# Performance work log

Measured on AMD Instinct MI355X. Metric: run time of the kernel, lower is better.

The kernel has to match this reference:

```python
import jax, jax.numpy as jnp
import numpy as np

B, S, E, H = 8, 512, 1024, 16
D = E // H  # head_dim = 64


def _rope_tables(seq_len, head_dim):
    inv_freq = 1.0 / (10000.0 ** (np.arange(0, head_dim, 2, dtype=np.float32) / head_dim))
    pos = np.arange(seq_len, dtype=np.float32)
    ang = np.einsum('i,j->ij', pos, inv_freq)  # [S, D/2]
    return jnp.asarray(np.cos(ang)), jnp.asarray(np.sin(ang))


def setup_inputs() -> dict:
    key = jax.random.key(0)
    ks = jax.random.split(key, 12)
    std = 1.0 / np.sqrt(E)
    inp = {
        'x_q': jax.random.normal(ks[0], (B, S, E), jnp.float32),
        'x_k': jax.random.normal(ks[1], (B, S, E), jnp.float32),
        'x_v': jax.random.normal(ks[2], (B, S, E), jnp.float32),
        'Wq': jax.random.normal(ks[3], (E, E), jnp.float32) * std,
        'bq': jnp.zeros((E,), jnp.float32),
        'Wk': jax.random.normal(ks[4], (E, E), jnp.float32) * std,
        'bk': jnp.zeros((E,), jnp.float32),
        'Wv': jax.random.normal(ks[5], (E, E), jnp.float32) * std,
        'bv': jnp.zeros((E,), jnp.float32),
        'Wo': jax.random.normal(ks[6], (E, E), jnp.float32) * std,
        'bo': jnp.zeros((E,), jnp.float32),
        'temperature': jnp.ones((), jnp.float32),
    }
    cos, sin = _rope_tables(S, D)
    inp['cos'] = cos
    inp['sin'] = sin
    return inp


def reference(x_q, x_k, x_v, Wq, bq, Wk, bk, Wv, bv, Wo, bo, temperature, cos, sin):
    b, s, e = x_q.shape
    h, d = H, D

    def proj(x, W, bias):
        # torch Linear: x @ W.T + b ; then split heads -> [b, h, s, d]
        y = jnp.einsum('bse,fe->bsf', x, W) + bias
        return y.reshape(b, s, h, d).transpose(0, 2, 1, 3)

    q = proj(x_q, Wq, bq)
    k = proj(x_k, Wk, bk)
    v = proj(x_v, Wv, bv)

    c = cos[:s]  # [s, d/2]
    sn = sin[:s]

    def rope(t):
        # interleaved pairing: view as [..., d/2, 2]
        t2 = t.reshape(b, h, s, d // 2, 2)
        t0, t1 = t2[..., 0], t2[..., 1]
        r = jnp.stack([t0 * c - t1 * sn, t0 * sn + t1 * c], axis=-1)
        return r.reshape(b, h, s, d)

    q = rope(q)
    k = rope(k)

    def l2norm(t):
        # torch F.normalize: x / max(||x||, eps)
        n = jnp.sqrt(jnp.sum(t * t, axis=-1, keepdims=True))
        return t / jnp.maximum(n, 1e-12)

    q = l2norm(q)
    k = l2norm(k)

    scores = jnp.einsum('bhqd,bhkd->bhqk', q, k) * temperature
    attn = jax.nn.softmax(scores, axis=-1)
    out = jnp.einsum('bhqk,bhkd->bhqd', attn, v)
    out = out.transpose(0, 2, 1, 3).reshape(b, s, e)
    return jnp.einsum('bse,fe->bsf', out, Wo) + bo
```

## Files before the change

kernel.cpp:

```cpp
#include <hip/hip_runtime.h>
#include <stdint.h>

#define DEV __device__ __forceinline__

typedef __bf16 bf16x8 __attribute__((ext_vector_type(8)));
typedef float f32x4 __attribute__((ext_vector_type(4)));
typedef unsigned short u16;
typedef u16 u16x8 __attribute__((ext_vector_type(8)));
typedef u16 u16x4 __attribute__((ext_vector_type(4)));
typedef __attribute__((address_space(3))) uint8_t lds8;
typedef __attribute__((address_space(1))) const uint8_t glb8;

constexpr int Bb = 8, Ss = 512, Ee = 1024, Hh = 16;
constexpr int BS = Bb * Ss;

DEV u16 f2bf(float f) {
  union { float f; uint32_t u; } v; v.f = f;
  return (u16)((v.u + 0x7FFFu + ((v.u >> 16) & 1u)) >> 16);
}
DEV bf16x8 ldsbf8(const u16* p) {
  u16x8 u = *(const u16x8*)p;
  return __builtin_bit_cast(bf16x8, u);
}
DEV f32x4 mfma16(bf16x8 a, bf16x8 b, f32x4 c) {
  return __builtin_amdgcn_mfma_f32_16x16x32_bf16(a, b, c, 0, 0, 0);
}

struct ConvArgs {
  const float* s[7];
  u16* d[7];
  int n[7];
};

__global__ __launch_bounds__(256) void convert_k(ConvArgs a) {
  int z = blockIdx.y;
  int base = (blockIdx.x * 256 + threadIdx.x) * 8;
  if (base >= a.n[z]) return;
  const float4* sp = (const float4*)(a.s[z] + base);
  float4 v0 = sp[0], v1 = sp[1];
  u16x8 o;
  o[0] = f2bf(v0.x); o[1] = f2bf(v0.y); o[2] = f2bf(v0.z); o[3] = f2bf(v0.w);
  o[4] = f2bf(v1.x); o[5] = f2bf(v1.y); o[6] = f2bf(v1.z); o[7] = f2bf(v1.w);
  *(u16x8*)(a.d[z] + base) = o;
}

DEV void gemm_main(const u16* __restrict__ A, const u16* __restrict__ W,
                   f32x4 (&acc)[4][4]) {
  constexpr int K = Ee;
  __shared__ u16 sA[2][128 * 32], sB[2][128 * 32];
  const int tid = threadIdx.x, lane = tid & 63, wid = tid >> 6;
  const int lr = lane & 15, lh = lane >> 4;
  const int m0 = blockIdx.x * 128, n0 = blockIdx.y * 128;
  const int wm = (wid >> 1) * 64, wn = (wid & 1) * 64;

  const u16* aSrc[2]; const u16* bSrc[2]; int ldsOff[2];
#pragma unroll
  for (int j = 0; j < 2; ++j) {
    int c0 = j * 256 + wid * 64;
    int c = c0 + lane;
    int q = c >> 3, sl = c & 7;
    int rp = sl ^ (q & 7);
    int r = q * 2 + (rp >> 2), p = rp & 3;
    aSrc[j] = A + (size_t)(m0 + r) * K + p * 8;
    bSrc[j] = W + (size_t)(n0 + r) * K + p * 8;
    ldsOff[j] = c0 * 8;
  }
  int offA[4], offB[4];
#pragma unroll
  for (int t = 0; t < 4; ++t) {
    int ra = wm + t * 16 + lr;
    offA[t] = (ra >> 1) * 64 + ((((ra & 1) << 2) | lh) ^ ((ra >> 1) & 7)) * 8;
    int rb = wn + t * 16 + lr;
    offB[t] = (rb >> 1) * 64 + ((((rb & 1) << 2) | lh) ^ ((rb >> 1) & 7)) * 8;
  }
#pragma unroll
  for (int a = 0; a < 4; ++a)
#pragma unroll
    for (int q = 0; q < 4; ++q) acc[a][q] = f32x4{0.f, 0.f, 0.f, 0.f};

#define GSTAGE(buf, k0_)                                                       \
  {                                                                            \
    _Pragma("unroll") for (int j = 0; j < 2; ++j) {                            \
      __builtin_amdgcn_global_load_lds((glb8*)(aSrc[j] + (k0_)),               \
                                       (lds8*)&sA[buf][ldsOff[j]], 16, 0, 0);  \
      __builtin_amdgcn_global_load_lds((glb8*)(bSrc[j] + (k0_)),               \
                                       (lds8*)&sB[buf][ldsOff[j]], 16, 0, 0);  \
    }                                                                          \
  }

  GSTAGE(0, 0);
  __syncthreads();
  int cur = 0;
  for (int k0 = 0; k0 < K; k0 += 32) {
    if (k0 + 32 < K) GSTAGE(cur ^ 1, k0 + 32);
    bf16x8 af[4], bfv[4];
#pragma unroll
    for (int t = 0; t < 4; ++t) {
      af[t] = ldsbf8(&sA[cur][offA[t]]);
      bfv[t] = ldsbf8(&sB[cur][offB[t]]);
    }
#pragma unroll
    for (int mt = 0; mt < 4; ++mt)
#pragma unroll
      for (int nt = 0; nt < 4; ++nt)
        acc[mt][nt] = mfma16(af[mt], bfv[nt], acc[mt][nt]);
    __syncthreads();
    cur ^= 1;
  }
#undef GSTAGE
}

__global__ __launch_bounds__(256) void gemm_qkv(
    const u16* xq, const u16* xk, const u16* xv,
    const u16* wq, const u16* wk, const u16* wv,
    const float* bq_, const float* bk_, const float* bv_,
    const float* __restrict__ cosT, const float* __restrict__ sinT,
    u16* qh, u16* kh, u16* vt) {
  int z = blockIdx.z;
  const u16* A = z == 0 ? xq : (z == 1 ? xk : xv);
  const u16* W = z == 0 ? wq : (z == 1 ? wk : wv);
  const float* bias = z == 0 ? bq_ : (z == 1 ? bk_ : bv_);
  f32x4 acc[4][4];
  gemm_main(A, W, acc);

  const int tid = threadIdx.x, lane = tid & 63, wid = tid >> 6;
  const int lr = lane & 15, lh = lane >> 4;
  const int m0 = blockIdx.x * 128, n0 = blockIdx.y * 128;
  const int wm = (wid >> 1) * 64, wn = (wid & 1) * 64;
  const int hh = (n0 + wn) >> 6;
  const int b = m0 >> 9;
  const int sbase = (m0 & 511) + wm;
  float bv[4];
#pragma unroll
  for (int nt = 0; nt < 4; ++nt) bv[nt] = bias[n0 + wn + nt * 16 + lr];

  if (z < 2) {
    u16* dst = z ? kh : qh;
#pragma unroll
    for (int mt = 0; mt < 4; ++mt) {
#pragma unroll
      for (int i = 0; i < 4; ++i) {
        int s = sbase + mt * 16 + lh * 4 + i;
        float r[4];
        float ss = 0.f;
#pragma unroll
        for (int nt = 0; nt < 4; ++nt) {
          float t = acc[mt][nt][i] + bv[nt];
          float pr = __shfl_xor(t, 1);
          int ii = (nt * 16 + lr) >> 1;
          float c = cosT[s * 32 + ii], sn = sinT[s * 32 + ii];
          r[nt] = (lane & 1) ? (pr * sn + t * c) : (t * c - pr * sn);
          ss += r[nt] * r[nt];
        }
#pragma unroll
        for (int m = 1; m < 16; m <<= 1) ss += __shfl_xor(ss, m);
        float inv = 1.f / fmaxf(sqrtf(ss), 1e-12f);
        size_t ob = ((size_t)(b * Hh + hh) * Ss + s) * 64;
#pragma unroll
        for (int nt = 0; nt < 4; ++nt) dst[ob + nt * 16 + lr] = f2bf(r[nt] * inv);
      }
    }
  } else {
#pragma unroll
    for (int mt = 0; mt < 4; ++mt) {
#pragma unroll
      for (int nt = 0; nt < 4; ++nt) {
        int d = nt * 16 + lr;
        int s4 = sbase + mt * 16 + lh * 4;
        u16x4 pv;
#pragma unroll
        for (int i = 0; i < 4; ++i) pv[i] = f2bf(acc[mt][nt][i] + bv[nt]);
        *(u16x4*)(vt + ((size_t)(b * Hh + hh) * 64 + d) * Ss + s4) = pv;
      }
    }
  }
}

__global__ __launch_bounds__(256) void gemm_fin(
    const u16* __restrict__ ctx, const u16* __restrict__ wo,
    const float* __restrict__ bo_, float* __restrict__ out) {
  f32x4 acc[4][4];
  gemm_main(ctx, wo, acc);
  const int tid = threadIdx.x, lane = tid & 63, wid = tid >> 6;
  const int lr = lane & 15, lh = lane >> 4;
  const int m0 = blockIdx.x * 128, n0 = blockIdx.y * 128;
  const int wm = (wid >> 1) * 64, wn = (wid & 1) * 64;
#pragma unroll
  for (int nt = 0; nt < 4; ++nt) {
    int col = n0 + wn + nt * 16 + lr;
    float bvv = bo_[col];
#pragma unroll
    for (int mt = 0; mt < 4; ++mt)
#pragma unroll
      for (int i = 0; i < 4; ++i) {
        int row = m0 + wm + mt * 16 + lh * 4 + i;
        out[(size_t)row * Ee + col] = acc[mt][nt][i] + bvv;
      }
  }
}

__global__ __launch_bounds__(256) void attn_k(
    const u16* __restrict__ qh, const u16* __restrict__ kh, const u16* __restrict__ vT,
    const float* __restrict__ temp, u16* __restrict__ ctx) {
  __shared__ u16 sQ[64 * 64], sK[2][64 * 64], sV[2][64 * 64];
  __shared__ u16 sP[4][16 * 64];
  int tid = threadIdx.x, lane = tid & 63, wid = tid >> 6;
  int lr = lane & 15, lh = lane >> 4;
  int qb = blockIdx.x, h = blockIdx.y, b = blockIdx.z;
  float T = temp[0];
  size_t bh = (size_t)b * Hh + h;
  const u16* Qg = qh + (bh * Ss + qb * 64) * 64;
  const u16* Kg = kh + bh * Ss * 64;
  const u16* Vg = vT + bh * 64 * Ss;

  const u16* qSrc[2]; const u16* kSrc[2]; const u16* vSrc[2]; int soff[2];
#pragma unroll
  for (int j = 0; j < 2; ++j) {
    int c0 = j * 256 + wid * 64;
    int c = c0 + lane;
    int r = c >> 3, p = (c & 7) ^ (r & 7);
    soff[j] = c0 * 8;
    qSrc[j] = Qg + r * 64 + p * 8;
    kSrc[j] = Kg + r * 64 + p * 8;
    vSrc[j] = Vg + (size_t)r * Ss + p * 8;
  }
#define ASTAGE(buf, kb_)                                                        \
  {                                                                             \
    _Pragma("unroll") for (int j = 0; j < 2; ++j) {                             \
      __builtin_amdgcn_global_load_lds((glb8*)(kSrc[j] + (kb_) * 4096),         \
                                       (lds8*)&sK[buf][soff[j]], 16, 0, 0);     \
      __builtin_amdgcn_global_load_lds((glb8*)(vSrc[j] + (kb_) * 64),           \
                                       (lds8*)&sV[buf][soff[j]], 16, 0, 0);     \
    }                                                                           \
  }

#pragma unroll
  for (int j = 0; j < 2; ++j)
    __builtin_amdgcn_global_load_lds((glb8*)qSrc[j], (lds8*)&sQ[soff[j]], 16, 0, 0);
  ASTAGE(0, 0);
  __syncthreads();

  bf16x8 qf[2];
  {
    int rq = wid * 16 + lr;
    qf[0] = ldsbf8(&sQ[rq * 64 + ((0 + lh) ^ (lr & 7)) * 8]);
    qf[1] = ldsbf8(&sQ[rq * 64 + ((4 + lh) ^ (lr & 7)) * 8]);
  }
  f32x4 o[4];
#pragma unroll
  for (int nt = 0; nt < 4; ++nt) o[nt] = f32x4{0.f, 0.f, 0.f, 0.f};
  float mrow[4] = {-1e30f, -1e30f, -1e30f, -1e30f};
  float lrow[4] = {0.f, 0.f, 0.f, 0.f};
  u16* sPw = sP[wid];
  int cur = 0;

  for (int kb = 0; kb < Ss / 64; ++kb) {
    if (kb + 1 < Ss / 64) ASTAGE(cur ^ 1, kb + 1);
    f32x4 sc[4];
#pragma unroll
    for (int nt = 0; nt < 4; ++nt) sc[nt] = f32x4{0.f, 0.f, 0.f, 0.f};
    __builtin_amdgcn_s_setprio(1);
#pragma unroll
    for (int ks = 0; ks < 2; ++ks)
#pragma unroll
      for (int nt = 0; nt < 4; ++nt) {
        int rk = nt * 16 + lr;
        bf16x8 kf = ldsbf8(&sK[cur][rk * 64 + ((ks * 4 + lh) ^ (lr & 7)) * 8]);
        sc[nt] = mfma16(qf[ks], kf, sc[nt]);
      }
    __builtin_amdgcn_s_setprio(0);
    float mb[4], mn[4], scl[4], psum[4];
#pragma unroll
    for (int nt = 0; nt < 4; ++nt)
#pragma unroll
      for (int i = 0; i < 4; ++i) sc[nt][i] *= T;
#pragma unroll
    for (int i = 0; i < 4; ++i) {
      mb[i] = fmaxf(fmaxf(sc[0][i], sc[1][i]), fmaxf(sc[2][i], sc[3][i]));
#pragma unroll
      for (int m = 1; m < 16; m <<= 1) mb[i] = fmaxf(mb[i], __shfl_xor(mb[i], m));
      mn[i] = fmaxf(mrow[i], mb[i]);
      scl[i] = __expf(mrow[i] - mn[i]);
      psum[i] = 0.f;
    }
#pragma unroll
    for (int nt = 0; nt < 4; ++nt)
#pragma unroll
      for (int i = 0; i < 4; ++i) {
        float p = __expf(sc[nt][i] - mn[i]);
        psum[i] += p;
        int kk = nt * 16 + lr;
        int rowp = lh * 4 + i;
        sPw[rowp * 64 + ((kk >> 3) ^ (rowp & 7)) * 8 + (kk & 7)] = f2bf(p);
      }
#pragma unroll
    for (int i = 0; i < 4; ++i) {
#pragma unroll
      for (int m = 1; m < 16; m <<= 1) psum[i] += __shfl_xor(psum[i], m);
      lrow[i] = lrow[i] * scl[i] + psum[i];
      mrow[i] = mn[i];
    }
#pragma unroll
    for (int nt = 0; nt < 4; ++nt)
#pragma unroll
      for (int i = 0; i < 4; ++i) o[nt][i] *= scl[i];
    __builtin_amdgcn_s_setprio(1);
#pragma unroll
    for (int ks = 0; ks < 2; ++ks) {
      bf16x8 pf = ldsbf8(&sPw[lr * 64 + ((ks * 4 + lh) ^ (lr & 7)) * 8]);
#pragma unroll
      for (int nt = 0; nt < 4; ++nt) {
        int dv = nt * 16 + lr;
        bf16x8 vf = ldsbf8(&sV[cur][dv * 64 + ((ks * 4 + lh) ^ (lr & 7)) * 8]);
        o[nt] = mfma16(pf, vf, o[nt]);
      }
    }
    __builtin_amdgcn_s_setprio(0);
    __syncthreads();
    cur ^= 1;
  }
#undef ASTAGE
#pragma unroll
  for (int nt = 0; nt < 4; ++nt) {
    int d = nt * 16 + lr;
#pragma unroll
    for (int i = 0; i < 4; ++i) {
      int row = qb * 64 + wid * 16 + lh * 4 + i;
      float val = o[nt][i] / lrow[i];
      ctx[((size_t)b * Ss + row) * Ee + h * 64 + d] = f2bf(val);
    }
  }
}

extern "C" void kernel_launch(void* const* d_in, const int* in_sizes, int n_in,
                              void* d_out, int out_size, void* d_ws, size_t ws_size,
                              hipStream_t stream) {
  const float* x_q = (const float*)d_in[0];
  const float* x_k = (const float*)d_in[1];
  const float* x_v = (const float*)d_in[2];
  const float* Wq = (const float*)d_in[3];
  const float* bq = (const float*)d_in[4];
  const float* Wk = (const float*)d_in[5];
  const float* bk = (const float*)d_in[6];
  const float* Wv = (const float*)d_in[7];
  const float* bv = (const float*)d_in[8];
  const float* Wo = (const float*)d_in[9];
  const float* bo = (const float*)d_in[10];
  const float* temp = (const float*)d_in[11];
  const float* cosT = (const float*)d_in[12];
  const float* sinT = (const float*)d_in[13];

  char* ws = (char*)d_ws;
  constexpr size_t MB = 1ull << 20;
  u16* XQb = (u16*)(ws + 0 * MB);
  u16* XKb = (u16*)(ws + 8 * MB);
  u16* XVb = (u16*)(ws + 16 * MB);
  u16* WOb = (u16*)(ws + 24 * MB);
  u16* QH  = (u16*)(ws + 26 * MB);
  u16* KH  = (u16*)(ws + 34 * MB);
  u16* VT  = (u16*)(ws + 42 * MB);
  u16* CTX = XKb;
  u16* WQb = (u16*)d_out;
  u16* WKb = (u16*)((char*)d_out + 2 * MB);
  u16* WVb = (u16*)((char*)d_out + 4 * MB);

  ConvArgs ca;
  ca.s[0] = x_q; ca.s[1] = x_k; ca.s[2] = x_v;
  ca.s[3] = Wq;  ca.s[4] = Wk;  ca.s[5] = Wv; ca.s[6] = Wo;
  ca.d[0] = XQb; ca.d[1] = XKb; ca.d[2] = XVb;
  ca.d[3] = WQb; ca.d[4] = WKb; ca.d[5] = WVb; ca.d[6] = WOb;
  int nx = BS * Ee, nw = Ee * Ee;
  ca.n[0] = nx; ca.n[1] = nx; ca.n[2] = nx;
  ca.n[3] = nw; ca.n[4] = nw; ca.n[5] = nw; ca.n[6] = nw;
  convert_k<<<dim3(nx / (256 * 8), 7), 256, 0, stream>>>(ca);

  gemm_qkv<<<dim3(BS / 128, Ee / 128, 3), 256, 0, stream>>>(
      XQb, XKb, XVb, WQb, WKb, WVb, bq, bk, bv, cosT, sinT, QH, KH, VT);
  attn_k<<<dim3(Ss / 64, Hh, Bb), 256, 0, stream>>>(QH, KH, VT, temp, CTX);
  gemm_fin<<<dim3(BS / 128, Ee / 128), 256, 0, stream>>>(CTX, WOb, bo, (float*)d_out);
}
```

Measured before the change: 220.5 us.

## Load attention K/V/Q fragments directly from global, drop LDS staging and barriers

The attention kernel no longer stages Q, K and V tiles into double-buffered shared memory. Each wave reads its MFMA fragments straight from global memory into registers, relying on L2/L1 caching, and the per-iteration block barrier is removed. The GEMM loop also moves its shared-memory fragment reads ahead of issuing the next async global-to-LDS stage. The attention change trades LDS traffic and synchronisation for redundant, less coalesced global loads across the four waves, with no prefetch overlap for K/V.

```diff
diff --git a/kernel.cpp b/kernel.cpp
--- a/kernel.cpp
+++ b/kernel.cpp
@@ -18,7 +18,7 @@
   union { float f; uint32_t u; } v; v.f = f;
   return (u16)((v.u + 0x7FFFu + ((v.u >> 16) & 1u)) >> 16);
 }
-DEV bf16x8 ldsbf8(const u16* p) {
+DEV bf16x8 ld8(const u16* p) {
   u16x8 u = *(const u16x8*)p;
   return __builtin_bit_cast(bf16x8, u);
 }
@@ -92,13 +92,13 @@
   __syncthreads();
   int cur = 0;
   for (int k0 = 0; k0 < K; k0 += 32) {
+    bf16x8 af[4], bfv[4];
+#pragma unroll
+    for (int t = 0; t < 4; ++t) {
+      af[t] = ld8(&sA[cur][offA[t]]);
+      bfv[t] = ld8(&sB[cur][offB[t]]);
+    }
     if (k0 + 32 < K) GSTAGE(cur ^ 1, k0 + 32);
-    bf16x8 af[4], bfv[4];
-#pragma unroll
-    for (int t = 0; t < 4; ++t) {
-      af[t] = ldsbf8(&sA[cur][offA[t]]);
-      bfv[t] = ldsbf8(&sB[cur][offB[t]]);
-    }
 #pragma unroll
     for (int mt = 0; mt < 4; ++mt)
 #pragma unroll
@@ -202,7 +202,6 @@
 __global__ __launch_bounds__(256) void attn_k(
     const u16* __restrict__ qh, const u16* __restrict__ kh, const u16* __restrict__ vT,
     const float* __restrict__ temp, u16* __restrict__ ctx) {
-  __shared__ u16 sQ[64 * 64], sK[2][64 * 64], sV[2][64 * 64];
   __shared__ u16 sP[4][16 * 64];
   int tid = threadIdx.x, lane = tid & 63, wid = tid >> 6;
   int lr = lane & 15, lh = lane >> 4;
@@ -213,49 +212,25 @@
   const u16* Kg = kh + bh * Ss * 64;
   const u16* Vg = vT + bh * 64 * Ss;
 
-  const u16* qSrc[2]; const u16* kSrc[2]; const u16* vSrc[2]; int soff[2];
-#pragma unroll
-  for (int j = 0; j < 2; ++j) {
-    int c0 = j * 256 + wid * 64;
-    int c = c0 + lane;
-    int r = c >> 3, p = (c & 7) ^ (r & 7);
-    soff[j] = c0 * 8;
-    qSrc[j] = Qg + r * 64 + p * 8;
-    kSrc[j] = Kg + r * 64 + p * 8;
-    vSrc[j] = Vg + (size_t)r * Ss + p * 8;
-  }
-#define ASTAGE(buf, kb_)                                                        \
-  {                                                                             \
-    _Pragma("unroll") for (int j = 0; j < 2; ++j) {                             \
-      __builtin_amdgcn_global_load_lds((glb8*)(kSrc[j] + (kb_) * 4096),         \
-                                       (lds8*)&sK[buf][soff[j]], 16, 0, 0);     \
-      __builtin_amdgcn_global_load_lds((glb8*)(vSrc[j] + (kb_) * 64),           \
-                                       (lds8*)&sV[buf][soff[j]], 16, 0, 0);     \
-    }                                                                           \
-  }
-
-#pragma unroll
-  for (int j = 0; j < 2; ++j)
-    __builtin_amdgcn_global_load_lds((glb8*)qSrc[j], (lds8*)&sQ[soff[j]], 16, 0, 0);
-  ASTAGE(0, 0);
-  __syncthreads();
-
+  const int rq = wid * 16 + lr;
   bf16x8 qf[2];
-  {
-    int rq = wid * 16 + lr;
-    qf[0] = ldsbf8(&sQ[rq * 64 + ((0 + lh) ^ (lr & 7)) * 8]);
-    qf[1] = ldsbf8(&sQ[rq * 64 + ((4 + lh) ^ (lr & 7)) * 8]);
-  }
+  qf[0] = ld8(Qg + rq * 64 + lh * 8);
+  qf[1] = ld8(Qg + rq * 64 + (4 + lh) * 8);
+
   f32x4 o[4];
 #pragma unroll
   for (int nt = 0; nt < 4; ++nt) o[nt] = f32x4{0.f, 0.f, 0.f, 0.f};
   float mrow[4] = {-1e30f, -1e30f, -1e30f, -1e30f};
   float lrow[4] = {0.f, 0.f, 0.f, 0.f};
   u16* sPw = sP[wid];
-  int cur = 0;
 
   for (int kb = 0; kb < Ss / 64; ++kb) {
-    if (kb + 1 < Ss / 64) ASTAGE(cur ^ 1, kb + 1);
+    bf16x8 kf[2][4];
+#pragma unroll
+    for (int ks = 0; ks < 2; ++ks)
+#pragma unroll
+      for (int nt = 0; nt < 4; ++nt)
+        kf[ks][nt] = ld8(Kg + (size_t)(kb * 64 + nt * 16 + lr) * 64 + (ks * 4 + lh) * 8);
     f32x4 sc[4];
 #pragma unroll
     for (int nt = 0; nt < 4; ++nt) sc[nt] = f32x4{0.f, 0.f, 0.f, 0.f};
@@ -263,12 +238,10 @@
 #pragma unroll
     for (int ks = 0; ks < 2; ++ks)
 #pragma unroll
-      for (int nt = 0; nt < 4; ++nt) {
-        int rk = nt * 16 + lr;
-        bf16x8 kf = ldsbf8(&sK[cur][rk * 64 + ((ks * 4 + lh) ^ (lr & 7)) * 8]);
-        sc[nt] = mfma16(qf[ks], kf, sc[nt]);
-      }
+      for (int nt = 0; nt < 4; ++nt)
+        sc[nt] = mfma16(qf[ks], kf[ks][nt], sc[nt]);
     __builtin_amdgcn_s_setprio(0);
+
     float mb[4], mn[4], scl[4], psum[4];
 #pragma unroll
     for (int nt = 0; nt < 4; ++nt)
@@ -304,22 +277,23 @@
     for (int nt = 0; nt < 4; ++nt)
 #pragma unroll
       for (int i = 0; i < 4; ++i) o[nt][i] *= scl[i];
+
+    bf16x8 vf[2][4];
+#pragma unroll
+    for (int ks = 0; ks < 2; ++ks)
+#pragma unroll
+      for (int nt = 0; nt < 4; ++nt)
+        vf[ks][nt] = ld8(Vg + (size_t)(nt * 16 + lr) * Ss + kb * 64 + (ks * 4 + lh) * 8);
     __builtin_amdgcn_s_setprio(1);
 #pragma unroll
     for (int ks = 0; ks < 2; ++ks) {
-      bf16x8 pf = ldsbf8(&sPw[lr * 64 + ((ks * 4 + lh) ^ (lr & 7)) * 8]);
-#pragma unroll
-      for (int nt = 0; nt < 4; ++nt) {
-        int dv = nt * 16 + lr;
-        bf16x8 vf = ldsbf8(&sV[cur][dv * 64 + ((ks * 4 + lh) ^ (lr & 7)) * 8]);
-        o[nt] = mfma16(pf, vf, o[nt]);
-      }
+      bf16x8 pf = ld8(&sPw[lr * 64 + ((ks * 4 + lh) ^ (lr & 7)) * 8]);
+#pragma unroll
+      for (int nt = 0; nt < 4; ++nt)
+        o[nt] = mfma16(pf, vf[ks][nt], o[nt]);
     }
     __builtin_amdgcn_s_setprio(0);
-    __syncthreads();
-    cur ^= 1;
-  }
-#undef ASTAGE
+  }
 #pragma unroll
   for (int nt = 0; nt < 4; ++nt) {
     int d = nt * 16 + lr;
```

Result: slower. 250.2 us (+13.5%).

## Replace full-drain syncs with vmcnt-gated double-buffer pipeline in GEMM and attention

Applied to the files above, without the earlier changes.

The GEMM and attention main loops are manually unrolled by two with fixed LDS buffer pointers. Each `__syncthreads` (which drains all outstanding loads) is replaced by `s_waitcnt vmcnt(N)` plus a raw barrier, so only the older stage must land before compute. The next stage's async loads are issued right after a buffer is consumed, keeping one stage of global->LDS traffic in flight during compute. This relies on in-order vmcnt counting matching the hard-coded wait counts, so any change to the number of loads per stage would silently break correctness.

```diff
diff --git a/kernel.cpp b/kernel.cpp
--- a/kernel.cpp
+++ b/kernel.cpp
@@ -18,13 +18,15 @@
   union { float f; uint32_t u; } v; v.f = f;
   return (u16)((v.u + 0x7FFFu + ((v.u >> 16) & 1u)) >> 16);
 }
-DEV bf16x8 ldsbf8(const u16* p) {
+DEV bf16x8 ld8(const u16* p) {
   u16x8 u = *(const u16x8*)p;
   return __builtin_bit_cast(bf16x8, u);
 }
 DEV f32x4 mfma16(bf16x8 a, bf16x8 b, f32x4 c) {
   return __builtin_amdgcn_mfma_f32_16x16x32_bf16(a, b, c, 0, 0, 0);
 }
+#define BAR() __builtin_amdgcn_s_barrier()
+#define WAITVM(VM) asm volatile("s_waitcnt vmcnt(" VM ")" ::: "memory")
 
 struct ConvArgs {
   const float* s[7];
@@ -78,36 +80,47 @@
 #pragma unroll
     for (int q = 0; q < 4; ++q) acc[a][q] = f32x4{0.f, 0.f, 0.f, 0.f};
 
-#define GSTAGE(buf, k0_)                                                       \
-  {                                                                            \
-    _Pragma("unroll") for (int j = 0; j < 2; ++j) {                            \
-      __builtin_amdgcn_global_load_lds((glb8*)(aSrc[j] + (k0_)),               \
-                                       (lds8*)&sA[buf][ldsOff[j]], 16, 0, 0);  \
-      __builtin_amdgcn_global_load_lds((glb8*)(bSrc[j] + (k0_)),               \
-                                       (lds8*)&sB[buf][ldsOff[j]], 16, 0, 0);  \
-    }                                                                          \
-  }
-
-  GSTAGE(0, 0);
-  __syncthreads();
-  int cur = 0;
-  for (int k0 = 0; k0 < K; k0 += 32) {
-    if (k0 + 32 < K) GSTAGE(cur ^ 1, k0 + 32);
+  auto gstage = [&](u16* dA, u16* dB, int k0) {
+#pragma unroll
+    for (int j = 0; j < 2; ++j) {
+      __builtin_amdgcn_global_load_lds((glb8*)(aSrc[j] + k0),
+                                       (lds8*)(dA + ldsOff[j]), 16, 0, 0);
+      __builtin_amdgcn_global_load_lds((glb8*)(bSrc[j] + k0),
+                                       (lds8*)(dB + ldsOff[j]), 16, 0, 0);
+    }
+  };
+  auto gbody = [&](const u16* sAs, const u16* sBs) {
     bf16x8 af[4], bfv[4];
 #pragma unroll
     for (int t = 0; t < 4; ++t) {
-      af[t] = ldsbf8(&sA[cur][offA[t]]);
-      bfv[t] = ldsbf8(&sB[cur][offB[t]]);
+      af[t] = ld8(&sAs[offA[t]]);
+      bfv[t] = ld8(&sBs[offB[t]]);
     }
 #pragma unroll
     for (int mt = 0; mt < 4; ++mt)
 #pragma unroll
       for (int nt = 0; nt < 4; ++nt)
         acc[mt][nt] = mfma16(af[mt], bfv[nt], acc[mt][nt]);
-    __syncthreads();
-    cur ^= 1;
-  }
-#undef GSTAGE
+  };
+
+  gstage(sA[0], sB[0], 0);
+  gstage(sA[1], sB[1], 32);
+  for (int p = 0; p < 15; ++p) {
+    int k0 = p * 64;
+    WAITVM("4"); BAR();
+    gbody(sA[0], sB[0]);
+    BAR();
+    gstage(sA[0], sB[0], k0 + 64);
+    WAITVM("4"); BAR();
+    gbody(sA[1], sB[1]);
+    BAR();
+    gstage(sA[1], sB[1], k0 + 96);
+  }
+  WAITVM("4"); BAR();
+  gbody(sA[0], sB[0]);
+  BAR();
+  WAITVM("0"); BAR();
+  gbody(sA[1], sB[1]);
 }
 
 __global__ __launch_bounds__(256) void gemm_qkv(
@@ -224,27 +237,27 @@
     kSrc[j] = Kg + r * 64 + p * 8;
     vSrc[j] = Vg + (size_t)r * Ss + p * 8;
   }
-#define ASTAGE(buf, kb_)                                                        \
-  {                                                                             \
-    _Pragma("unroll") for (int j = 0; j < 2; ++j) {                             \
-      __builtin_amdgcn_global_load_lds((glb8*)(kSrc[j] + (kb_) * 4096),         \
-                                       (lds8*)&sK[buf][soff[j]], 16, 0, 0);     \
-      __builtin_amdgcn_global_load_lds((glb8*)(vSrc[j] + (kb_) * 64),           \
-                                       (lds8*)&sV[buf][soff[j]], 16, 0, 0);     \
-    }                                                                           \
-  }
+  auto astage = [&](u16* dK, u16* dV, int kb) {
+#pragma unroll
+    for (int j = 0; j < 2; ++j) {
+      __builtin_amdgcn_global_load_lds((glb8*)(kSrc[j] + kb * 4096),
+                                       (lds8*)(dK + soff[j]), 16, 0, 0);
+      __builtin_amdgcn_global_load_lds((glb8*)(vSrc[j] + kb * 64),
+                                       (lds8*)(dV + soff[j]), 16, 0, 0);
+    }
+  };
 
 #pragma unroll
   for (int j = 0; j < 2; ++j)
     __builtin_amdgcn_global_load_lds((glb8*)qSrc[j], (lds8*)&sQ[soff[j]], 16, 0, 0);
-  ASTAGE(0, 0);
-  __syncthreads();
-
+  astage(sK[0], sV[0], 0);
+  astage(sK[1], sV[1], 1);
+  WAITVM("8"); BAR();
   bf16x8 qf[2];
   {
     int rq = wid * 16 + lr;
-    qf[0] = ldsbf8(&sQ[rq * 64 + ((0 + lh) ^ (lr & 7)) * 8]);
-    qf[1] = ldsbf8(&sQ[rq * 64 + ((4 + lh) ^ (lr & 7)) * 8]);
+    qf[0] = ld8(&sQ[rq * 64 + ((0 + lh) ^ (lr & 7)) * 8]);
+    qf[1] = ld8(&sQ[rq * 64 + ((4 + lh) ^ (lr & 7)) * 8]);
   }
   f32x4 o[4];
 #pragma unroll
@@ -252,10 +265,8 @@
   float mrow[4] = {-1e30f, -1e30f, -1e30f, -1e30f};
   float lrow[4] = {0.f, 0.f, 0.f, 0.f};
   u16* sPw = sP[wid];
-  int cur = 0;
-
-  for (int kb = 0; kb < Ss / 64; ++kb) {
-    if (kb + 1 < Ss / 64) ASTAGE(cur ^ 1, kb + 1);
+
+  auto kvstep = [&](const u16* sKs, const u16* sVs) {
     f32x4 sc[4];
 #pragma unroll
     for (int nt = 0; nt < 4; ++nt) sc[nt] = f32x4{0.f, 0.f, 0.f, 0.f};
@@ -265,7 +276,7 @@
 #pragma unroll
       for (int nt = 0; nt < 4; ++nt) {
         int rk = nt * 16 + lr;
-        bf16x8 kf = ldsbf8(&sK[cur][rk * 64 + ((ks * 4 + lh) ^ (lr & 7)) * 8]);
+        bf16x8 kf = ld8(&sKs[rk * 64 + ((ks * 4 + lh) ^ (lr & 7)) * 8]);
         sc[nt] = mfma16(qf[ks], kf, sc[nt]);
       }
     __builtin_amdgcn_s_setprio(0);
@@ -307,19 +318,33 @@
     __builtin_amdgcn_s_setprio(1);
 #pragma unroll
     for (int ks = 0; ks < 2; ++ks) {
-      bf16x8 pf = ldsbf8(&sPw[lr * 64 + ((ks * 4 + lh) ^ (lr & 7)) * 8]);
+      bf16x8 pf = ld8(&sPw[lr * 64 + ((ks * 4 + lh) ^ (lr & 7)) * 8]);
 #pragma unroll
       for (int nt = 0; nt < 4; ++nt) {
         int dv = nt * 16 + lr;
-        bf16x8 vf = ldsbf8(&sV[cur][dv * 64 + ((ks * 4 + lh) ^ (lr & 7)) * 8]);
+        bf16x8 vf = ld8(&sVs[dv * 64 + ((ks * 4 + lh) ^ (lr & 7)) * 8]);
         o[nt] = mfma16(pf, vf, o[nt]);
       }
     }
     __builtin_amdgcn_s_setprio(0);
-    __syncthreads();
-    cur ^= 1;
-  }
-#undef ASTAGE
+  };
+
+  for (int p = 0; p < 3; ++p) {
+    WAITVM("4"); BAR();
+    kvstep(sK[0], sV[0]);
+    BAR();
+    astage(sK[0], sV[0], 2 * p + 2);
+    WAITVM("4"); BAR();
+    kvstep(sK[1], sV[1]);
+    BAR();
+    astage(sK[1], sV[1], 2 * p + 3);
+  }
+  WAITVM("4"); BAR();
+  kvstep(sK[0], sV[0]);
+  BAR();
+  WAITVM("0"); BAR();
+  kvstep(sK[1], sV[1]);
+
 #pragma unroll
   for (int nt = 0; nt < 4; ++nt) {
     int d = nt * 16 + lr;
```

After: 230.5 us. 4.5% more time.
